# Kernel optimization log

Measured on AMD Instinct MI355X. Metric: run time of the kernel, lower is better.

## Reference

```python
import jax, jax.numpy as jnp
import numpy as np

IN_CAPS, IN_SIZE = 2401, 8
OUT_CAPS, OUT_SIZE = 8, 16
ROUTING_ITERS = 3


def squash(s, axis):
    mag_sq = jnp.sum(s * s, axis=axis, keepdims=True)
    mag = jnp.sqrt(mag_sq)
    return mag_sq / (1.0 + mag_sq) * (s / mag)


def setup_inputs() -> dict:
    key = jax.random.key(0)
    kx, kw = jax.random.split(key)
    B = 256
    x = jax.random.normal(kx, (B, IN_CAPS, IN_SIZE), dtype=jnp.float32)
    stdv = 1.0 / np.sqrt(IN_CAPS)
    W = jax.random.uniform(kw, (IN_CAPS, OUT_CAPS, OUT_SIZE, IN_SIZE),
                           dtype=jnp.float32, minval=-stdv, maxval=stdv)
    return {"x": x, "W": W}


def reference(x, W):
    # u_hat[b,i,o,c] = W[i,o,c,d] @ x[b,i,d]   -> [B, 2401, 8, 16]
    u_hat = jnp.einsum('iocd,bid->bioc', W, x)
    u_hat_det = jax.lax.stop_gradient(u_hat)

    b_ij = jnp.zeros((IN_CAPS, OUT_CAPS), dtype=x.dtype)
    v_j = None
    for it in range(ROUTING_ITERS):
        c_ij = jax.nn.softmax(b_ij, axis=1)  # softmax over out_capsules
        last = (it == ROUTING_ITERS - 1)
        u = u_hat if last else u_hat_det
        s_j = jnp.einsum('io,bioc->boc', c_ij, u)  # [B, 8, 16]
        v_j = squash(s_j, axis=-1)
        if not last:
            # agreement: mean over batch of <u_hat_i, v_j>
            a = jnp.einsum('bioc,boc->io', u_hat_det, v_j) / x.shape[0]
            b_ij = b_ij + a
    return v_j  # [B, 8, 16]
```

## Files before the change

kernel.cpp:

```cpp
#include <hip/hip_runtime.h>
#include <math.h>

#define IC     2401
#define BSZ    256
#define OC     8
#define CS     16
#define OCC    128
#define XROW   19208
#define KP     19264
#define KTILES 301
#define NI     128

typedef __attribute__((ext_vector_type(8))) short short8;
typedef __attribute__((ext_vector_type(4))) float f32x4;

__device__ __forceinline__ unsigned short f2bf(float f) {
    union { float f; unsigned u; } v; v.f = f;
    const unsigned r = v.u + 0x7FFF + ((v.u >> 16) & 1);
    return (unsigned short)(r >> 16);
}
__device__ __forceinline__ float bf2f(unsigned short h) {
    union { unsigned u; float f; } v; v.u = ((unsigned)h) << 16;
    return v.f;
}

__global__ __launch_bounds__(256)
void prep_kernel(const float* __restrict__ x, const float* __restrict__ W,
                 unsigned short* __restrict__ xT, unsigned short* __restrict__ xB,
                 unsigned short* __restrict__ Wbf, unsigned short* __restrict__ cwt)
{
    const int tid = threadIdx.x;
    if (blockIdx.x < 1204) {
        __shared__ float Ts[64 * 65];
        const int bg = blockIdx.x & 3;
        const int kt = blockIdx.x >> 2;
#pragma unroll
        for (int r = 0; r < 4; ++r) {
            const int flat = r * 256 + tid;
            const int b = flat >> 4, cq = flat & 15;
            const int col = kt * 64 + cq * 4;
            float4 v = make_float4(0.f, 0.f, 0.f, 0.f);
            if (col < XROW) v = *(const float4*)(x + (size_t)(bg * 64 + b) * XROW + col);
            *(float4*)&Ts[b * 65 + cq * 4] = v;
        }
        __syncthreads();
#pragma unroll
        for (int r = 0; r < 2; ++r) {
            const int flat = r * 256 + tid;
            const int rl = flat >> 3, bq = flat & 7;
            union { short8 v; unsigned short h[8]; } o;
#pragma unroll
            for (int j = 0; j < 8; ++j) o.h[j] = f2bf(Ts[(bq * 8 + j) * 65 + rl]);
            *(short8*)(xT + (size_t)(kt * 64 + rl) * 256 + bg * 64 + bq * 8) = o.v;
        }
#pragma unroll
        for (int r = 0; r < 2; ++r) {
            const int flat = r * 256 + tid;
            const int b = flat >> 3, g = flat & 7;
            union { short8 v; unsigned short h[8]; } o;
#pragma unroll
            for (int j = 0; j < 8; ++j) o.h[j] = f2bf(Ts[b * 65 + g * 8 + j]);
            *(short8*)(xB + (size_t)(bg * 64 + b) * KP + (size_t)kt * 64 + g * 8) = o.v;
        }
    } else {
        __shared__ float Ws[8 * 1032];
        const int i0 = (blockIdx.x - 1204) * 8;
#pragma unroll
        for (int r = 0; r < 8; ++r) {
            const int flat = r * 256 + tid;
            const int g = flat >> 8, rem = flat & 255;
            int gi = i0 + g; if (gi > 2400) gi = 2400;
            const float4 v = *(const float4*)(W + (size_t)gi * 1024 + rem * 4);
            *(float4*)&Ws[g * 1032 + rem * 4] = v;
        }
        __syncthreads();
#pragma unroll
        for (int r = 0; r < 4; ++r) {
            const int flat = r * 256 + tid;
            const int oc = flat >> 3, g = flat & 7;
            const int gi = i0 + g;
            union { short8 v; unsigned short h[8]; } w, c;
            if (gi <= 2400) {
                const float* wp = &Ws[g * 1032 + oc * 8];
#pragma unroll
                for (int j = 0; j < 8; ++j) {
                    w.h[j] = f2bf(wp[j]);
                    c.h[j] = f2bf(0.125f * wp[j]);
                }
            } else {
#pragma unroll
                for (int j = 0; j < 8; ++j) { w.h[j] = 0; c.h[j] = 0; }
            }
            *(short8*)(Wbf + (size_t)oc * KP + (size_t)gi * 8) = w.v;
            *(short8*)(cwt + (size_t)oc * KP + (size_t)gi * 8) = c.v;
        }
    }
}

__global__ __launch_bounds__(256, 2)
void s_gemm(const unsigned short* __restrict__ xB, const unsigned short* __restrict__ cwt,
            float* __restrict__ spart)
{
    __shared__ __align__(16) unsigned short Xs[64 * 64];
    __shared__ __align__(16) unsigned short Bs[128 * 64];
    const int tid = threadIdx.x;
    const int bg  = blockIdx.x, iy = blockIdx.y;
    const int b0  = bg * 64;
    const int ln  = tid & 63;
    const int mr  = ln & 15, qd = ln >> 4;
    const int mh  = (tid >> 6) & 1;
    const int nh  = tid >> 7;

    f32x4 acc[2][4];
#pragma unroll
    for (int a = 0; a < 2; ++a)
#pragma unroll
        for (int b = 0; b < 4; ++b) acc[a][b] = (f32x4){0.f, 0.f, 0.f, 0.f};

    const int srow = tid >> 3, scol = tid & 7;
    const int ssw  = (scol ^ (srow & 7)) * 8;
    const unsigned short* xp0 = xB  + (size_t)(b0 + srow) * KP + (size_t)scol * 8;
    const unsigned short* bp0 = cwt + (size_t)srow * KP + (size_t)scol * 8;

    short8 vx[2], vb[4];
    int kt = iy;
#pragma unroll
    for (int r = 0; r < 2; ++r) vx[r] = *(const short8*)(xp0 + (size_t)r * 32 * KP + (size_t)kt * 64);
#pragma unroll
    for (int r = 0; r < 4; ++r) vb[r] = *(const short8*)(bp0 + (size_t)r * 32 * KP + (size_t)kt * 64);

    while (true) {
        __syncthreads();
#pragma unroll
        for (int r = 0; r < 2; ++r) *(short8*)&Xs[(r * 32 + srow) * 64 + ssw] = vx[r];
#pragma unroll
        for (int r = 0; r < 4; ++r) *(short8*)&Bs[(r * 32 + srow) * 64 + ssw] = vb[r];
        const int ktn = kt + NI;
        if (ktn < KTILES) {
#pragma unroll
            for (int r = 0; r < 2; ++r) vx[r] = *(const short8*)(xp0 + (size_t)r * 32 * KP + (size_t)ktn * 64);
#pragma unroll
            for (int r = 0; r < 4; ++r) vb[r] = *(const short8*)(bp0 + (size_t)r * 32 * KP + (size_t)ktn * 64);
        }
        __syncthreads();
#pragma unroll
        for (int kk = 0; kk < 2; ++kk) {
            const int csw = ((kk * 4 + qd) ^ (mr & 7)) * 8;
            const short8 a0 = *(const short8*)&Xs[(mh * 32 + mr) * 64 + csw];
            const short8 a1 = *(const short8*)&Xs[(mh * 32 + 16 + mr) * 64 + csw];
#pragma unroll
            for (int nt = 0; nt < 4; ++nt) {
                const short8 b = *(const short8*)&Bs[(nh * 64 + nt * 16 + mr) * 64 + csw];
                acc[0][nt] = __builtin_amdgcn_mfma_f32_16x16x32_bf16(a0, b, acc[0][nt], 0, 0, 0);
                acc[1][nt] = __builtin_amdgcn_mfma_f32_16x16x32_bf16(a1, b, acc[1][nt], 0, 0, 0);
            }
        }
        if (ktn >= KTILES) break;
        kt = ktn;
    }

    float* op = spart + ((size_t)iy * BSZ + b0) * OCC;
#pragma unroll
    for (int mt = 0; mt < 2; ++mt)
#pragma unroll
        for (int nt = 0; nt < 4; ++nt)
#pragma unroll
            for (int r = 0; r < 4; ++r)
                op[(size_t)(mh * 32 + mt * 16 + qd * 4 + r) * OCC + nh * 64 + nt * 16 + mr]
                    = acc[mt][nt][r];
}

__global__ __launch_bounds__(256)
void squash_kernel(const float* __restrict__ spart, float* __restrict__ vout,
                   unsigned short* __restrict__ vT, int writeT)
{
    __shared__ float red[256];
    const int tid = threadIdx.x;
    const int r0  = blockIdx.x * 8;
    const int idx = tid & 127;
    const int k0  = tid >> 7;

    const float* base = spart + (size_t)r0 * 16 + idx;
    float acc = 0.0f;
#pragma unroll 8
    for (int k = k0; k < NI; k += 2) acc += base[(size_t)k * (BSZ * OCC)];
    red[tid] = acc;
    __syncthreads();

    if (tid < 128) {
        const float s = red[tid] + red[tid + 128];
        float ms = s * s;
        ms += __shfl_xor(ms, 1); ms += __shfl_xor(ms, 2);
        ms += __shfl_xor(ms, 4); ms += __shfl_xor(ms, 8);
        const float scale = sqrtf(ms) / (1.0f + ms);
        const float outv = s * scale;
        const int row = r0 + (tid >> 4);
        const int j   = tid & 15;
        if (writeT) {
            vT[(size_t)((row & 7) * 16 + j) * 256 + (row >> 3)] = f2bf(outv);
        } else {
            vout[(size_t)row * 16 + j] = outv;
        }
    }
}

template<bool FIRST>
__global__ __launch_bounds__(256, 2)
void a_gemm(const unsigned short* __restrict__ xT, const unsigned short* __restrict__ vT,
            const unsigned short* __restrict__ Wbf, float* __restrict__ bij,
            unsigned short* __restrict__ cwt)
{
    __shared__ __align__(16) char smraw[128 * 68 * 4];
    unsigned short* As = (unsigned short*)smraw;
    unsigned short* Bx = (unsigned short*)(smraw + 16384);
    float* Hs = (float*)smraw;

    const int tid = threadIdx.x;
    const int i0  = blockIdx.x * 8;
    const int ln  = tid & 63, wv = tid >> 6;
    const int mr  = ln & 15, qd = ln >> 4;

    f32x4 acc[2][4];
#pragma unroll
    for (int a = 0; a < 2; ++a)
#pragma unroll
        for (int b = 0; b < 4; ++b) acc[a][b] = (f32x4){0.f, 0.f, 0.f, 0.f};

    const int srow = tid >> 3, scol = tid & 7;
    const int ssw  = (scol ^ (srow & 7)) * 8;
    const unsigned short* ap0 = vT + (size_t)srow * 256 + (size_t)scol * 8;
    const unsigned short* bp0 = xT + (size_t)(i0 * 8 + srow) * 256 + (size_t)scol * 8;

    short8 va[4], vbx[2];
#pragma unroll
    for (int r = 0; r < 4; ++r) va[r]  = *(const short8*)(ap0 + (size_t)r * 32 * 256);
#pragma unroll
    for (int r = 0; r < 2; ++r) vbx[r] = *(const short8*)(bp0 + (size_t)r * 32 * 256);

    for (int bc = 0; bc < 4; ++bc) {
        __syncthreads();
#pragma unroll
        for (int r = 0; r < 4; ++r) *(short8*)&As[(r * 32 + srow) * 64 + ssw] = va[r];
#pragma unroll
        for (int r = 0; r < 2; ++r) *(short8*)&Bx[(r * 32 + srow) * 64 + ssw] = vbx[r];
        if (bc < 3) {
#pragma unroll
            for (int r = 0; r < 4; ++r) va[r]  = *(const short8*)(ap0 + (size_t)r * 32 * 256 + (bc + 1) * 64);
#pragma unroll
            for (int r = 0; r < 2; ++r) vbx[r] = *(const short8*)(bp0 + (size_t)r * 32 * 256 + (bc + 1) * 64);
        }
        __syncthreads();
#pragma unroll
        for (int kk = 0; kk < 2; ++kk) {
            const int csw = ((kk * 4 + qd) ^ (mr & 7)) * 8;
#pragma unroll
            for (int nt = 0; nt < 4; ++nt) {
                const short8 b = *(const short8*)&Bx[(nt * 16 + mr) * 64 + csw];
#pragma unroll
                for (int mt = 0; mt < 2; ++mt) {
                    const short8 a = *(const short8*)&As[((wv * 2 + mt) * 16 + mr) * 64 + csw];
                    acc[mt][nt] = __builtin_amdgcn_mfma_f32_16x16x32_bf16(a, b, acc[mt][nt], 0, 0, 0);
                }
            }
        }
    }

    __syncthreads();
#pragma unroll
    for (int mt = 0; mt < 2; ++mt)
#pragma unroll
        for (int nt = 0; nt < 4; ++nt)
#pragma unroll
            for (int r = 0; r < 4; ++r)
                Hs[((wv * 2 + mt) * 16 + qd * 4 + r) * 68 + nt * 16 + mr] = acc[mt][nt][r];
    __syncthreads();

    const int ch = tid & 3, oo = (tid >> 2) & 7, il = tid >> 5;
    const int ival = i0 + il;
    const int gi = (ival < IC) ? ival : IC - 1;
    const unsigned short* Wt = Wbf + (size_t)(oo * 16 + ch * 4) * KP + (size_t)gi * 8;

    float wreg[4][8];
#pragma unroll
    for (int c = 0; c < 4; ++c) {
        union { short8 v; unsigned short h[8]; } uw;
        uw.v = *(const short8*)(Wt + (size_t)c * KP);
#pragma unroll
        for (int j = 0; j < 8; ++j) wreg[c][j] = bf2f(uw.h[j]);
    }
    float p = 0.0f;
#pragma unroll
    for (int c = 0; c < 4; ++c) {
        const float* hr = &Hs[(oo * 16 + ch * 4 + c) * 68 + il * 8];
        const float4 h0 = *(const float4*)hr;
        const float4 h1 = *(const float4*)(hr + 4);
        p = fmaf(wreg[c][0], h0.x, p); p = fmaf(wreg[c][1], h0.y, p);
        p = fmaf(wreg[c][2], h0.z, p); p = fmaf(wreg[c][3], h0.w, p);
        p = fmaf(wreg[c][4], h1.x, p); p = fmaf(wreg[c][5], h1.y, p);
        p = fmaf(wreg[c][6], h1.z, p); p = fmaf(wreg[c][7], h1.w, p);
    }
    p += __shfl_xor(p, 1); p += __shfl_xor(p, 2);
    const float anew = p * (1.0f / 256.0f);
    float bv = anew;
    if (!FIRST) bv += bij[gi * 8 + oo];
    float mx = bv;
    mx = fmaxf(mx, __shfl_xor(mx, 4));
    mx = fmaxf(mx, __shfl_xor(mx, 8));
    mx = fmaxf(mx, __shfl_xor(mx, 16));
    const float e = expf(bv - mx);
    float ss = e;
    ss += __shfl_xor(ss, 4); ss += __shfl_xor(ss, 8); ss += __shfl_xor(ss, 16);
    float cv = e / ss;
    if (ival >= IC) cv = 0.0f;
    if (ch == 0 && ival < IC) bij[ival * 8 + oo] = bv;
#pragma unroll
    for (int c = 0; c < 4; ++c) {
        union { short8 v; unsigned short h[8]; } o;
#pragma unroll
        for (int j = 0; j < 8; ++j) o.h[j] = f2bf(cv * wreg[c][j]);
        *(short8*)(cwt + (size_t)(oo * 16 + ch * 4 + c) * KP + (size_t)ival * 8) = o.v;
    }
}

extern "C" void kernel_launch(void* const* d_in, const int* in_sizes, int n_in,
                              void* d_out, int out_size, void* d_ws, size_t ws_size,
                              hipStream_t stream)
{
    const float* x = (const float*)d_in[0];
    const float* W = (const float*)d_in[1];
    float* out = (float*)d_out;

    char* p = (char*)d_ws;
    float*          spart = (float*)p;          p += (size_t)NI * BSZ * OCC * 4;
    unsigned short* xT    = (unsigned short*)p; p += (size_t)KP * 256 * 2;
    unsigned short* xB    = (unsigned short*)p; p += (size_t)256 * KP * 2;
    unsigned short* Wbf   = (unsigned short*)p; p += (size_t)128 * KP * 2;
    unsigned short* cwt   = (unsigned short*)p; p += (size_t)128 * KP * 2;
    unsigned short* vT    = (unsigned short*)p; p += (size_t)128 * 256 * 2;
    float*          bij   = (float*)p;

    const dim3 sgrid(4, NI);

    prep_kernel<<<1505, 256, 0, stream>>>(x, W, xT, xB, Wbf, cwt);

    s_gemm<<<sgrid, 256, 0, stream>>>(xB, cwt, spart);
    squash_kernel<<<256, 256, 0, stream>>>(spart, nullptr, vT, 1);
    a_gemm<true><<<KTILES, 256, 0, stream>>>(xT, vT, Wbf, bij, cwt);
    s_gemm<<<sgrid, 256, 0, stream>>>(xB, cwt, spart);
    squash_kernel<<<256, 256, 0, stream>>>(spart, nullptr, vT, 1);
    a_gemm<false><<<KTILES, 256, 0, stream>>>(xT, vT, Wbf, bij, cwt);
    s_gemm<<<sgrid, 256, 0, stream>>>(xB, cwt, spart);
    squash_kernel<<<256, 256, 0, stream>>>(spart, out, vT, 0);
}
```

Baseline: 141.3 us.

## Replace split-K partial buffer with atomic accumulation and fuse squash into a_gemm

The s_gemm split-K reduction now accumulates directly into a zeroed fp32 buffer with atomic adds, and the split factor drops from 128 to 32. The separate squash kernels between iterations are removed: a_gemm recomputes the squash of s from the accumulated buffer while staging its A tile, and a small squash_out kernel writes the final output. This removes two kernel launches and the large partial-sum write and read traffic, at the cost of atomic contention, a redundant squash in every a_gemm block, and fewer s_gemm blocks for parallelism.

```diff
diff --git a/kernel.cpp b/kernel.cpp
--- a/kernel.cpp
+++ b/kernel.cpp
@@ -9,7 +9,7 @@
 #define XROW   19208
 #define KP     19264
 #define KTILES 301
-#define NI     128
+#define SNI    32
 
 typedef __attribute__((ext_vector_type(8))) short short8;
 typedef __attribute__((ext_vector_type(4))) float f32x4;
@@ -23,13 +23,23 @@
     union { unsigned u; float f; } v; v.u = ((unsigned)h) << 16;
     return v.f;
 }
+__device__ __forceinline__ void atomAddF32(float* p, float v) {
+    (void)__hip_atomic_fetch_add(p, v, __ATOMIC_RELAXED, __HIP_MEMORY_SCOPE_AGENT);
+}
 
 __global__ __launch_bounds__(256)
 void prep_kernel(const float* __restrict__ x, const float* __restrict__ W,
                  unsigned short* __restrict__ xT, unsigned short* __restrict__ xB,
-                 unsigned short* __restrict__ Wbf, unsigned short* __restrict__ cwt)
+                 unsigned short* __restrict__ Wbf, unsigned short* __restrict__ cwt,
+                 float* __restrict__ s_acc_all)
 {
     const int tid = threadIdx.x;
+    if (blockIdx.x < 3) {
+        float4* z = (float4*)(s_acc_all + (size_t)blockIdx.x * BSZ * OCC);
+#pragma unroll
+        for (int r = 0; r < 32; ++r)
+            z[r * 256 + tid] = make_float4(0.f, 0.f, 0.f, 0.f);
+    }
     if (blockIdx.x < 1204) {
         __shared__ float Ts[64 * 65];
         const int bg = blockIdx.x & 3;
@@ -99,7 +109,7 @@
 
 __global__ __launch_bounds__(256, 2)
 void s_gemm(const unsigned short* __restrict__ xB, const unsigned short* __restrict__ cwt,
-            float* __restrict__ spart)
+            float* __restrict__ s_acc)
 {
     __shared__ __align__(16) unsigned short Xs[64 * 64];
     __shared__ __align__(16) unsigned short Bs[128 * 64];
@@ -135,7 +145,7 @@
         for (int r = 0; r < 2; ++r) *(short8*)&Xs[(r * 32 + srow) * 64 + ssw] = vx[r];
 #pragma unroll
         for (int r = 0; r < 4; ++r) *(short8*)&Bs[(r * 32 + srow) * 64 + ssw] = vb[r];
-        const int ktn = kt + NI;
+        const int ktn = kt + SNI;
         if (ktn < KTILES) {
 #pragma unroll
             for (int r = 0; r < 2; ++r) vx[r] = *(const short8*)(xp0 + (size_t)r * 32 * KP + (size_t)ktn * 64);
@@ -159,54 +169,20 @@
         kt = ktn;
     }
 
-    float* op = spart + ((size_t)iy * BSZ + b0) * OCC;
+    float* op = s_acc + (size_t)b0 * OCC;
 #pragma unroll
     for (int mt = 0; mt < 2; ++mt)
 #pragma unroll
         for (int nt = 0; nt < 4; ++nt)
 #pragma unroll
             for (int r = 0; r < 4; ++r)
-                op[(size_t)(mh * 32 + mt * 16 + qd * 4 + r) * OCC + nh * 64 + nt * 16 + mr]
-                    = acc[mt][nt][r];
-}
-
-__global__ __launch_bounds__(256)
-void squash_kernel(const float* __restrict__ spart, float* __restrict__ vout,
-                   unsigned short* __restrict__ vT, int writeT)
-{
-    __shared__ float red[256];
-    const int tid = threadIdx.x;
-    const int r0  = blockIdx.x * 8;
-    const int idx = tid & 127;
-    const int k0  = tid >> 7;
-
-    const float* base = spart + (size_t)r0 * 16 + idx;
-    float acc = 0.0f;
-#pragma unroll 8
-    for (int k = k0; k < NI; k += 2) acc += base[(size_t)k * (BSZ * OCC)];
-    red[tid] = acc;
-    __syncthreads();
-
-    if (tid < 128) {
-        const float s = red[tid] + red[tid + 128];
-        float ms = s * s;
-        ms += __shfl_xor(ms, 1); ms += __shfl_xor(ms, 2);
-        ms += __shfl_xor(ms, 4); ms += __shfl_xor(ms, 8);
-        const float scale = sqrtf(ms) / (1.0f + ms);
-        const float outv = s * scale;
-        const int row = r0 + (tid >> 4);
-        const int j   = tid & 15;
-        if (writeT) {
-            vT[(size_t)((row & 7) * 16 + j) * 256 + (row >> 3)] = f2bf(outv);
-        } else {
-            vout[(size_t)row * 16 + j] = outv;
-        }
-    }
+                atomAddF32(&op[(size_t)(mh * 32 + mt * 16 + qd * 4 + r) * OCC
+                               + nh * 64 + nt * 16 + mr], acc[mt][nt][r]);
 }
 
 template<bool FIRST>
 __global__ __launch_bounds__(256, 2)
-void a_gemm(const unsigned short* __restrict__ xT, const unsigned short* __restrict__ vT,
+void a_gemm(const unsigned short* __restrict__ xT, const float* __restrict__ s_acc,
             const unsigned short* __restrict__ Wbf, float* __restrict__ bij,
             unsigned short* __restrict__ cwt)
 {
@@ -228,24 +204,44 @@
 
     const int srow = tid >> 3, scol = tid & 7;
     const int ssw  = (scol ^ (srow & 7)) * 8;
-    const unsigned short* ap0 = vT + (size_t)srow * 256 + (size_t)scol * 8;
     const unsigned short* bp0 = xT + (size_t)(i0 * 8 + srow) * 256 + (size_t)scol * 8;
 
-    short8 va[4], vbx[2];
-#pragma unroll
-    for (int r = 0; r < 4; ++r) va[r]  = *(const short8*)(ap0 + (size_t)r * 32 * 256);
+    short8 vbx[2];
 #pragma unroll
     for (int r = 0; r < 2; ++r) vbx[r] = *(const short8*)(bp0 + (size_t)r * 32 * 256);
 
     for (int bc = 0; bc < 4; ++bc) {
         __syncthreads();
-#pragma unroll
-        for (int r = 0; r < 4; ++r) *(short8*)&As[(r * 32 + srow) * 64 + ssw] = va[r];
+        {
+            const int rr0 = tid * 2;
+#pragma unroll
+            for (int rv = 0; rv < 2; ++rv) {
+                const int rr = rr0 + rv;
+                const int bl = rr & 63;
+                const int o  = rr >> 6;
+                const float* sp = s_acc + (size_t)(bc * 64 + bl) * OCC + o * 16;
+                const float4 s0 = *(const float4*)(sp);
+                const float4 s1 = *(const float4*)(sp + 4);
+                const float4 s2 = *(const float4*)(sp + 8);
+                const float4 s3 = *(const float4*)(sp + 12);
+                float ms = s0.x*s0.x + s0.y*s0.y + s0.z*s0.z + s0.w*s0.w
+                         + s1.x*s1.x + s1.y*s1.y + s1.z*s1.z + s1.w*s1.w
+                         + s2.x*s2.x + s2.y*s2.y + s2.z*s2.z + s2.w*s2.w
+                         + s3.x*s3.x + s3.y*s3.y + s3.z*s3.z + s3.w*s3.w;
+                const float scale = sqrtf(ms) / (1.0f + ms);
+                float vv[16] = { s0.x, s0.y, s0.z, s0.w, s1.x, s1.y, s1.z, s1.w,
+                                 s2.x, s2.y, s2.z, s2.w, s3.x, s3.y, s3.z, s3.w };
+                const int blq = bl >> 3, blr = bl & 7;
+#pragma unroll
+                for (int c = 0; c < 16; ++c) {
+                    const int oc = o * 16 + c;
+                    As[oc * 64 + ((blq ^ (oc & 7)) * 8) + blr] = f2bf(vv[c] * scale);
+                }
+            }
+        }
 #pragma unroll
         for (int r = 0; r < 2; ++r) *(short8*)&Bx[(r * 32 + srow) * 64 + ssw] = vbx[r];
         if (bc < 3) {
-#pragma unroll
-            for (int r = 0; r < 4; ++r) va[r]  = *(const short8*)(ap0 + (size_t)r * 32 * 256 + (bc + 1) * 64);
 #pragma unroll
             for (int r = 0; r < 2; ++r) vbx[r] = *(const short8*)(bp0 + (size_t)r * 32 * 256 + (bc + 1) * 64);
         }
@@ -322,6 +318,27 @@
     }
 }
 
+__global__ __launch_bounds__(256)
+void squash_out(const float* __restrict__ s_acc, float* __restrict__ out)
+{
+    const int row = blockIdx.x * 256 + threadIdx.x;
+    const float* sp = s_acc + (size_t)(row >> 3) * OCC + (row & 7) * 16;
+    const float4 s0 = *(const float4*)(sp);
+    const float4 s1 = *(const float4*)(sp + 4);
+    const float4 s2 = *(const float4*)(sp + 8);
+    const float4 s3 = *(const float4*)(sp + 12);
+    const float ms = s0.x*s0.x + s0.y*s0.y + s0.z*s0.z + s0.w*s0.w
+                   + s1.x*s1.x + s1.y*s1.y + s1.z*s1.z + s1.w*s1.w
+                   + s2.x*s2.x + s2.y*s2.y + s2.z*s2.z + s2.w*s2.w
+                   + s3.x*s3.x + s3.y*s3.y + s3.z*s3.z + s3.w*s3.w;
+    const float scale = sqrtf(ms) / (1.0f + ms);
+    float4* op = (float4*)(out + (size_t)row * 16);
+    op[0] = make_float4(s0.x*scale, s0.y*scale, s0.z*scale, s0.w*scale);
+    op[1] = make_float4(s1.x*scale, s1.y*scale, s1.z*scale, s1.w*scale);
+    op[2] = make_float4(s2.x*scale, s2.y*scale, s2.z*scale, s2.w*scale);
+    op[3] = make_float4(s3.x*scale, s3.y*scale, s3.z*scale, s3.w*scale);
+}
+
 extern "C" void kernel_launch(void* const* d_in, const int* in_sizes, int n_in,
                               void* d_out, int out_size, void* d_ws, size_t ws_size,
                               hipStream_t stream)
@@ -331,24 +348,25 @@
     float* out = (float*)d_out;
 
     char* p = (char*)d_ws;
-    float*          spart = (float*)p;          p += (size_t)NI * BSZ * OCC * 4;
+    float*          s_acc = (float*)p;          p += (size_t)3 * BSZ * OCC * 4;
     unsigned short* xT    = (unsigned short*)p; p += (size_t)KP * 256 * 2;
     unsigned short* xB    = (unsigned short*)p; p += (size_t)256 * KP * 2;
     unsigned short* Wbf   = (unsigned short*)p; p += (size_t)128 * KP * 2;
     unsigned short* cwt   = (unsigned short*)p; p += (size_t)128 * KP * 2;
-    unsigned short* vT    = (unsigned short*)p; p += (size_t)128 * 256 * 2;
     float*          bij   = (float*)p;
 
-    const dim3 sgrid(4, NI);
-
-    prep_kernel<<<1505, 256, 0, stream>>>(x, W, xT, xB, Wbf, cwt);
-
-    s_gemm<<<sgrid, 256, 0, stream>>>(xB, cwt, spart);
-    squash_kernel<<<256, 256, 0, stream>>>(spart, nullptr, vT, 1);
-    a_gemm<true><<<KTILES, 256, 0, stream>>>(xT, vT, Wbf, bij, cwt);
-    s_gemm<<<sgrid, 256, 0, stream>>>(xB, cwt, spart);
-    squash_kernel<<<256, 256, 0, stream>>>(spart, nullptr, vT, 1);
-    a_gemm<false><<<KTILES, 256, 0, stream>>>(xT, vT, Wbf, bij, cwt);
-    s_gemm<<<sgrid, 256, 0, stream>>>(xB, cwt, spart);
-    squash_kernel<<<256, 256, 0, stream>>>(spart, out, vT, 0);
-}
+    float* s0 = s_acc;
+    float* s1 = s_acc + (size_t)BSZ * OCC;
+    float* s2 = s_acc + (size_t)2 * BSZ * OCC;
+
+    const dim3 sgrid(4, SNI);
+
+    prep_kernel<<<1505, 256, 0, stream>>>(x, W, xT, xB, Wbf, cwt, s_acc);
+
+    s_gemm<<<sgrid, 256, 0, stream>>>(xB, cwt, s0);
+    a_gemm<true><<<KTILES, 256, 0, stream>>>(xT, s0, Wbf, bij, cwt);
+    s_gemm<<<sgrid, 256, 0, stream>>>(xB, cwt, s1);
+    a_gemm<false><<<KTILES, 256, 0, stream>>>(xT, s1, Wbf, bij, cwt);
+    s_gemm<<<sgrid, 256, 0, stream>>>(xB, cwt, s2);
+    squash_out<<<8, 256, 0, stream>>>(s2, out);
+}
```

After: 138.9 us. No clear change (-1.7%).
